# Optimization experiments

Measured on AMD Instinct MI355X. Metric: run time of the kernel, lower is better.

The kernel has to match this reference:

```python
import jax, jax.numpy as jnp
import numpy as np

LOC_SIZE, CID_SIZE, UID_SIZE, TIM_SIZE = 10000, 300, 1000, 48
LOC_EMB, CID_EMB, UID_EMB, TIM_EMB = 256, 64, 64, 32
HID, ENC_HID = 500, 250            # hidden_size, history_hidden_size
SEQ, TGT = 2048, 256
INPUT = LOC_EMB + TIM_EMB + CID_EMB  # 352


def setup_inputs() -> dict:
    key = jax.random.key(0)
    ks = jax.random.split(key, 32)
    n = lambda i, shape, s=0.05: (jax.random.normal(ks[i], shape, dtype=jnp.float32) * s)
    d = {}
    d["loc"] = jax.random.randint(ks[0], (SEQ, 1), 0, LOC_SIZE)
    d["tim"] = jax.random.randint(ks[1], (SEQ, 1), 0, TIM_SIZE)
    d["cid"] = jax.random.randint(ks[2], (SEQ, 1), 0, CID_SIZE)
    d["uid"] = jax.random.randint(ks[3], (1,), 0, UID_SIZE)
    d["target"] = jax.random.randint(ks[4], (TGT, 1), 0, LOC_SIZE)
    d["target_len"] = TGT
    d["time_sim_matrix"] = jax.random.uniform(ks[5], (TIM_SIZE, TIM_SIZE), dtype=jnp.float32)
    # keep distances away from 0 since the model computes 1/dist
    d["poi_distance_matrix"] = jax.random.uniform(ks[6], (LOC_SIZE, LOC_SIZE), dtype=jnp.float32, minval=0.1, maxval=2.0)
    d["poi_cid_tim"] = jax.random.uniform(ks[7], (TIM_SIZE, CID_SIZE), dtype=jnp.float32)
    # embedding tables (emb_loc/emb_cid are pretrained+frozen in the original)
    d["weight"] = n(8, (LOC_SIZE, LOC_EMB))
    d["weight_cid"] = n(9, (CID_SIZE, CID_EMB))
    d["emb_uid_w"] = n(10, (UID_SIZE, UID_EMB))
    d["emb_tim_w"] = n(11, (TIM_SIZE, TIM_EMB))
    # bidirectional encoder LSTM (hidden 250), gate order i,f,g,o like torch
    d["enc_Wih_f"] = n(12, (4 * ENC_HID, INPUT))
    d["enc_Whh_f"] = n(13, (4 * ENC_HID, ENC_HID))
    d["enc_b_f"] = jnp.zeros((4 * ENC_HID,), jnp.float32)
    d["enc_Wih_b"] = n(14, (4 * ENC_HID, INPUT))
    d["enc_Whh_b"] = n(15, (4 * ENC_HID, ENC_HID))
    d["enc_b_b"] = jnp.zeros((4 * ENC_HID,), jnp.float32)
    # decoder LSTM (hidden 500)
    d["dec_Wih"] = n(16, (4 * HID, INPUT))
    d["dec_Whh"] = n(17, (4 * HID, HID))
    d["dec_b"] = jnp.zeros((4 * HID,), jnp.float32)
    # linear layers
    d["fc_user_w"] = n(18, (HID, UID_EMB))
    d["fc_user_b"] = jnp.zeros((HID,), jnp.float32)
    d["fc_final_w"] = n(19, (LOC_SIZE, 3 * HID))
    d["fc_final_b"] = jnp.zeros((LOC_SIZE,), jnp.float32)
    d["fc_final2_w"] = n(20, (HID, 3 * HID))
    d["fc_final2_b"] = jnp.zeros((HID,), jnp.float32)
    return d


def _lstm(x, Wih, Whh, b, H):
    """Single-layer LSTM, batch=1. x: [T, D] -> hs: [T, H]."""
    h0 = jnp.zeros((H,), x.dtype)
    c0 = jnp.zeros((H,), x.dtype)

    def step(carry, xt):
        h, c = carry
        z = Wih @ xt + Whh @ h + b
        i, f, g, o = jnp.split(z, 4)
        c = jax.nn.sigmoid(f) * c + jax.nn.sigmoid(i) * jnp.tanh(g)
        h = jax.nn.sigmoid(o) * jnp.tanh(c)
        return (h, c), h

    _, hs = jax.lax.scan(step, (h0, c0), x)
    return hs


def _table_attn(history, current, table, invert=False, causal=False):
    """Vectorized replacement for the nested-loop lookup attention.
    energies[i, j] = table[current[i], history[j]] (or its reciprocal),
    upper triangle left at 0 for the self-attn variants (as in the original),
    then softmax over the full row (torch F.softmax default dim=1 on 2D)."""
    e = table[current[:, None], history[None, :]]
    if invert:
        e = 1.0 / e
    if causal:
        nn_ = e.shape[0]
        e = jnp.where(jnp.tril(jnp.ones((nn_, nn_), bool)), e, jnp.zeros((), e.dtype))
    return jax.nn.softmax(e, axis=-1)


def reference(loc, tim, cid, uid, target, target_len,
              time_sim_matrix, poi_distance_matrix, poi_cid_tim,
              weight, weight_cid, emb_uid_w, emb_tim_w,
              enc_Wih_f, enc_Whh_f, enc_b_f, enc_Wih_b, enc_Whh_b, enc_b_b,
              dec_Wih, dec_Whh, dec_b,
              fc_user_w, fc_user_b, fc_final_w, fc_final_b, fc_final2_w, fc_final2_b):
    T = int(target_len)
    loc_f, tim_f, cid_f = loc[:, 0], tim[:, 0], cid[:, 0]

    # cross attention: current window attends to history via lookup tables
    attn_cid_time = _table_attn(cid_f[:-T], tim_f[-T:], poi_cid_tim)
    attn_loc = _table_attn(loc_f[:-T], loc_f[-T:], poi_distance_matrix, invert=True)
    attn_time = _table_attn(tim_f[:-T], tim_f[-T:], time_sim_matrix)
    # self attention on the current window (lower-triangular fill)
    self_cid_time = _table_attn(cid_f[-T:], tim_f[-T:], poi_cid_tim, causal=True)
    self_loc = _table_attn(loc_f[-T:], loc_f[-T:], poi_distance_matrix, invert=True, causal=True)
    self_time = _table_attn(tim_f[-T:], tim_f[-T:], time_sim_matrix, causal=True)

    # embeddings (dropout is identity in eval)
    x = jnp.concatenate([weight[loc_f], emb_tim_w[tim_f], weight_cid[cid_f]], axis=1)  # [SEQ, INPUT]
    hist_x, tgt_x = x[:-T], x[-T:]

    # bidirectional encoder over history
    hf = _lstm(hist_x, enc_Wih_f, enc_Whh_f, enc_b_f, ENC_HID)
    hb = _lstm(hist_x[::-1], enc_Wih_b, enc_Whh_b, enc_b_b, ENC_HID)[::-1]
    hidden_history = jnp.concatenate([hf, hb], axis=1)  # [SEQ-T, 2*ENC_HID=500]

    # decoder over current window
    hidden_state = _lstm(tgt_x, dec_Wih, dec_Whh, dec_b, HID)  # [T, 500]

    target_emb = weight[target[:, 0]]  # [T, LOC_EMB]

    uid_emb = emb_uid_w[uid] @ fc_user_w.T + fc_user_b  # [1, 500]
    user_attn = jax.nn.softmax(uid_emb @ hidden_history.T, axis=-1)  # [1, hist]
    context_user = user_attn @ hidden_history  # [1, 500]

    context = (attn_loc + attn_time + attn_cid_time) @ hidden_history  # [T, 500]
    hidden_state = (self_loc + self_time + self_cid_time) @ hidden_state  # [T, 500]

    hidden_state_all = hidden_state + uid_emb  # broadcast of repeat
    out = jnp.concatenate([hidden_state_all, context,
                           jnp.broadcast_to(context_user, (T, HID))], axis=1)  # [T, 1500]
    y = out @ fc_final_w.T + fc_final_b    # [T, LOC_SIZE]
    y1 = out @ fc_final2_w.T + fc_final2_b  # [T, HID]
    score = jax.nn.log_softmax(y, axis=-1)
    return score, y1, target_emb
```

## Files before the change

### kernel.cpp

```cpp
#include <hip/hip_runtime.h>
#include <stdint.h>

#define HIST 1792
#define TGT 256
#define SEQ 2048
#define INPUT 352
#define EHID 250
#define HID 500

typedef _Float16 h2_t __attribute__((ext_vector_type(2)));

static __device__ __forceinline__ float fdot2(uint32_t a, uint32_t b, float c) {
  return __builtin_amdgcn_fdot2(__builtin_bit_cast(h2_t, a),
                                __builtin_bit_cast(h2_t, b), c, false);
}
static __device__ __forceinline__ uint32_t packh2(float lo, float hi) {
  h2_t h; h[0] = (_Float16)lo; h[1] = (_Float16)hi;
  return __builtin_bit_cast(uint32_t, h);
}
static __device__ __forceinline__ uint4 packq(const float* p) {
  uint4 r;
  r.x = packh2(p[0], p[1]); r.y = packh2(p[2], p[3]);
  r.z = packh2(p[4], p[5]); r.w = packh2(p[6], p[7]);
  return r;
}
static __device__ __forceinline__ float dotq(uint4 w, uint4 h, float acc) {
  acc = fdot2(w.x, h.x, acc); acc = fdot2(w.y, h.y, acc);
  acc = fdot2(w.z, h.z, acc); acc = fdot2(w.w, h.w, acc);
  return acc;
}
static __device__ __forceinline__ float sigf(float x) {
  x = fminf(fmaxf(x, -30.f), 30.f);
  return 1.f / (1.f + __expf(-x));
}
static __device__ __forceinline__ float tanh_f(float x) {
  x = fminf(fmaxf(x, -15.f), 15.f);
  float e = __expf(2.f * x);
  return (e - 1.f) / (e + 1.f);
}
static __device__ __forceinline__ void spin_flag(volatile int* f) {
  while (__hip_atomic_load(f, __ATOMIC_ACQUIRE, __HIP_MEMORY_SCOPE_AGENT) == 0)
    __builtin_amdgcn_s_sleep(2);
}
#define AW(dst, src) asm("v_accvgpr_write_b32 %0, %1" : "=a"(dst) : "v"(src))
#define AR(dst, src) asm("v_accvgpr_read_b32 %0, %1" : "=v"(dst) : "a"(src))
#define ARQ(dst, arr, base) do { AR(dst.x, arr[(base)+0]); AR(dst.y, arr[(base)+1]); AR(dst.z, arr[(base)+2]); AR(dst.w, arr[(base)+3]); } while(0)

__global__ void k_embed(const int* __restrict__ loc, const int* __restrict__ tim,
                        const int* __restrict__ cid, const int* __restrict__ target,
                        const float* __restrict__ weight, const float* __restrict__ emb_tim_w,
                        const float* __restrict__ weight_cid,
                        float* __restrict__ x, float* __restrict__ te) {
  int t = blockIdx.x, tid = threadIdx.x;
  if (t < SEQ) {
    int l = loc[t], tm = tim[t], cd = cid[t];
    float* xr = x + (size_t)t * INPUT;
    for (int k = tid; k < 256; k += blockDim.x) xr[k] = weight[(size_t)l * 256 + k];
    for (int k = tid; k < 32; k += blockDim.x)  xr[256 + k] = emb_tim_w[tm * 32 + k];
    for (int k = tid; k < 64; k += blockDim.x)  xr[288 + k] = weight_cid[cd * 64 + k];
  } else {
    int i = t - SEQ;
    int tg = target[i];
    for (int k = tid; k < 256; k += blockDim.x) te[(size_t)i * 256 + k] = weight[(size_t)tg * 256 + k];
  }
}

__global__ void k_gemm_t(const float* __restrict__ A, int lda,
                         const float* __restrict__ W, const float* __restrict__ bias,
                         float* __restrict__ C, int ldc,
                         int M, int N, int K, int revA) {
  __shared__ float As[16][65];
  __shared__ float Ws[16][65];
  const int bn = blockIdx.x * 64, bm = blockIdx.y * 64;
  const int tid = threadIdx.x;
  const int tx = tid & 15, ty = tid >> 4;
  float acc[4][4] = {};
  for (int k0 = 0; k0 < K; k0 += 16) {
    for (int i = tid; i < 1024; i += 256) {
      int m = i >> 4, k = i & 15;
      int gm = bm + m, gk = k0 + k;
      float v = 0.f;
      if (gm < M && gk < K) { int am = revA ? (M - 1 - gm) : gm; v = A[(size_t)am * lda + gk]; }
      As[k][m] = v;
    }
    for (int i = tid; i < 1024; i += 256) {
      int n = i >> 4, k = i & 15;
      int gn = bn + n, gk = k0 + k;
      float v = 0.f;
      if (gn < N && gk < K) v = W[(size_t)gn * K + gk];
      Ws[k][n] = v;
    }
    __syncthreads();
#pragma unroll
    for (int k = 0; k < 16; k++) {
      float a0 = As[k][ty * 4 + 0], a1 = As[k][ty * 4 + 1], a2 = As[k][ty * 4 + 2], a3 = As[k][ty * 4 + 3];
      float b0 = Ws[k][tx * 4 + 0], b1 = Ws[k][tx * 4 + 1], b2 = Ws[k][tx * 4 + 2], b3 = Ws[k][tx * 4 + 3];
      acc[0][0] += a0 * b0; acc[0][1] += a0 * b1; acc[0][2] += a0 * b2; acc[0][3] += a0 * b3;
      acc[1][0] += a1 * b0; acc[1][1] += a1 * b1; acc[1][2] += a1 * b2; acc[1][3] += a1 * b3;
      acc[2][0] += a2 * b0; acc[2][1] += a2 * b1; acc[2][2] += a2 * b2; acc[2][3] += a2 * b3;
      acc[3][0] += a3 * b0; acc[3][1] += a3 * b1; acc[3][2] += a3 * b2; acc[3][3] += a3 * b3;
    }
    __syncthreads();
  }
  for (int i = 0; i < 4; i++) {
    int gm = bm + ty * 4 + i; if (gm >= M) continue;
    for (int j = 0; j < 4; j++) {
      int gn = bn + tx * 4 + j; if (gn >= N) continue;
      C[(size_t)gm * ldc + gn] = acc[i][j] + (bias ? bias[gn] : 0.f);
    }
  }
}

__global__ void k_gemm_nn(const float* __restrict__ A, int lda,
                          const float* __restrict__ B, int ldb,
                          const float* __restrict__ addvec,
                          float* __restrict__ C, int ldc,
                          int M, int N, int K) {
  __shared__ float As[16][65];
  __shared__ float Bs[16][65];
  const int bn = blockIdx.x * 64, bm = blockIdx.y * 64;
  const int tid = threadIdx.x;
  const int tx = tid & 15, ty = tid >> 4;
  float acc[4][4] = {};
  for (int k0 = 0; k0 < K; k0 += 16) {
    for (int i = tid; i < 1024; i += 256) {
      int m = i >> 4, k = i & 15;
      int gm = bm + m, gk = k0 + k;
      float v = 0.f;
      if (gm < M && gk < K) v = A[(size_t)gm * lda + gk];
      As[k][m] = v;
    }
    for (int i = tid; i < 1024; i += 256) {
      int k = i >> 6, n = i & 63;
      int gk = k0 + k, gn = bn + n;
      float v = 0.f;
      if (gk < K && gn < N) v = B[(size_t)gk * ldb + gn];
      Bs[k][n] = v;
    }
    __syncthreads();
#pragma unroll
    for (int k = 0; k < 16; k++) {
      float a0 = As[k][ty * 4 + 0], a1 = As[k][ty * 4 + 1], a2 = As[k][ty * 4 + 2], a3 = As[k][ty * 4 + 3];
      float b0 = Bs[k][tx * 4 + 0], b1 = Bs[k][tx * 4 + 1], b2 = Bs[k][tx * 4 + 2], b3 = Bs[k][tx * 4 + 3];
      acc[0][0] += a0 * b0; acc[0][1] += a0 * b1; acc[0][2] += a0 * b2; acc[0][3] += a0 * b3;
      acc[1][0] += a1 * b0; acc[1][1] += a1 * b1; acc[1][2] += a1 * b2; acc[1][3] += a1 * b3;
      acc[2][0] += a2 * b0; acc[2][1] += a2 * b1; acc[2][2] += a2 * b2; acc[2][3] += a2 * b3;
      acc[3][0] += a3 * b0; acc[3][1] += a3 * b1; acc[3][2] += a3 * b2; acc[3][3] += a3 * b3;
    }
    __syncthreads();
  }
  for (int i = 0; i < 4; i++) {
    int gm = bm + ty * 4 + i; if (gm >= M) continue;
    for (int j = 0; j < 4; j++) {
      int gn = bn + tx * 4 + j; if (gn >= N) continue;
      C[(size_t)gm * ldc + gn] = acc[i][j] + (addvec ? addvec[gn] : 0.f);
    }
  }
}

#define WQL 12
#define WBYTES (WQL * 512 * 16)
__launch_bounds__(512)
__global__ void k_lstm(const float* __restrict__ A_f, const float* __restrict__ A_b,
                       const float* __restrict__ A_d,
                       const float* __restrict__ Whh_f, const float* __restrict__ Whh_b,
                       const float* __restrict__ Whh_d,
                       float* __restrict__ hh, float* __restrict__ hdec,
                       float* zpub, uint32_t* hpub, int* flag_z, int* flag_h) {
  const int b = blockIdx.x;
  const int tid = threadIdx.x;
  __shared__ __align__(16) unsigned char smem[WBYTES + 2048 + 4096];
  uint4* wl = (uint4*)smem;
  uint4* hbuf = (uint4*)(smem + WBYTES);
  float* zbuf = (float*)(smem + WBYTES + 2048);

  if (tid < 128) hbuf[tid] = make_uint4(0, 0, 0, 0);

  if (b < 2) {
    const float* A = (b == 0) ? A_f : A_b;
    const float* Whh = (b == 0) ? Whh_f : Whh_b;
    const bool act = tid < 500;
    uint4 wv0[10], wv1[10];
    uint32_t wa[128];
    if (act) {
      const float* wr0 = Whh + (size_t)tid * EHID;
      const float* wr1 = Whh + (size_t)(tid + 500) * EHID;
#pragma unroll
      for (int q = 0; q < 6; q++) {
        float t0[8], t1[8];
#pragma unroll
        for (int cc = 0; cc < 8; cc++) {
          int col = 208 + 8 * q + cc;
          t0[cc] = (col < EHID) ? wr0[col] : 0.f;
          t1[cc] = (col < EHID) ? wr1[col] : 0.f;
        }
        wl[(q * 2 + 0) * 512 + tid] = packq(t0);
        wl[(q * 2 + 1) * 512 + tid] = packq(t1);
      }
#pragma unroll
      for (int k = 0; k < 16; k++) {
        uint4 p0 = packq(wr0 + 8 * (10 + k));
        uint4 p1 = packq(wr1 + 8 * (10 + k));
        AW(wa[k * 4 + 0], p0.x); AW(wa[k * 4 + 1], p0.y);
        AW(wa[k * 4 + 2], p0.z); AW(wa[k * 4 + 3], p0.w);
        AW(wa[64 + k * 4 + 0], p1.x); AW(wa[64 + k * 4 + 1], p1.y);
        AW(wa[64 + k * 4 + 2], p1.z); AW(wa[64 + k * 4 + 3], p1.w);
      }
#pragma unroll
      for (int q = 0; q < 10; q++) { wv0[q] = packq(wr0 + 8 * q); wv1[q] = packq(wr1 + 8 * q); }
    }
    float c = 0.f;
    float aA = act ? A[tid] : 0.f;
    float aB = act ? A[500 + tid] : 0.f;
    __syncthreads();
    for (int t = 0; t < HIST; t++) {
      const uint4* hb = hbuf + (t & 1) * 32;
      if (act) {
        float z0 = aA, z1 = aB, y0 = 0.f, y1 = 0.f;
        int tn = (t + 1 < HIST) ? t + 1 : t;
        aA = A[tn * 1000 + tid];
        aB = A[tn * 1000 + 500 + tid];
#pragma unroll
        for (int q = 0; q < 10; q++) {
          uint4 hq = hb[q];
          z0 = dotq(wv0[q], hq, z0);
          z1 = dotq(wv1[q], hq, z1);
        }
#pragma unroll
        for (int k = 0; k < 16; k++) {
          uint4 hq = hb[10 + k];
          uint4 u0, u1;
          ARQ(u0, wa, k * 4);
          ARQ(u1, wa, 64 + k * 4);
          y0 = dotq(u0, hq, y0);
          y1 = dotq(u1, hq, y1);
        }
#pragma unroll
        for (int q = 0; q < 6; q++) {
          uint4 hq = hb[26 + q];
          z0 = dotq(wl[(q * 2 + 0) * 512 + tid], hq, z0);
          z1 = dotq(wl[(q * 2 + 1) * 512 + tid], hq, z1);
        }
        zbuf[tid] = z0 + y0;
        zbuf[500 + tid] = z1 + y1;
      }
      __syncthreads();
      float hval = 0.f;
      if (tid < EHID) {
        float zi = zbuf[tid], zf = zbuf[250 + tid], zg = zbuf[500 + tid], zo = zbuf[750 + tid];
        c = sigf(zf) * c + sigf(zi) * tanh_f(zg);
        hval = sigf(zo) * tanh_f(c);
        if (b == 0) hh[(size_t)t * HID + tid] = hval;
        else        hh[(size_t)(HIST - 1 - t) * HID + EHID + tid] = hval;
      }
      float hother = __shfl_xor(hval, 1);
      uint32_t* hw = (uint32_t*)(hbuf + ((t + 1) & 1) * 32);
      if (tid < EHID && !(tid & 1)) hw[tid >> 1] = packh2(hval, hother);
      __syncthreads();
    }
  } else {
    const int gi = b - 2;
    const int j = tid;
    const bool act = (j < 500);
    uint4 wv[20];
    uint32_t wa[128];
    if (act) {
      const float* wr = Whh_d + (size_t)(gi * 500 + j) * HID;
#pragma unroll
      for (int q = 0; q < 12; q++) {
        float tmp[8];
#pragma unroll
        for (int cc = 0; cc < 8; cc++) {
          int col = 416 + 8 * q + cc;
          tmp[cc] = (col < HID) ? wr[col] : 0.f;
        }
        wl[q * 512 + tid] = packq(tmp);
      }
#pragma unroll
      for (int k = 0; k < 32; k++) {
        uint4 pq = packq(wr + 8 * (20 + k));
        AW(wa[k * 4 + 0], pq.x); AW(wa[k * 4 + 1], pq.y);
        AW(wa[k * 4 + 2], pq.z); AW(wa[k * 4 + 3], pq.w);
      }
#pragma unroll
      for (int q = 0; q < 20; q++) wv[q] = packq(wr + 8 * q);
    }
    uint32_t* hdd = (uint32_t*)hbuf;
    float c = 0.f;
    float aD = act ? A_d[gi * 500 + j] : 0.f;
    __syncthreads();
    for (int t = 0; t < TGT; t++) {
      const uint4* hb = hbuf + (t & 1) * 64;
      float z = 0.f;
      if (act) {
        float z0 = aD, z1 = 0.f, z2 = 0.f, z3 = 0.f;
        int tn = (t + 1 < TGT) ? t + 1 : t;
        aD = A_d[tn * 2000 + gi * 500 + j];
#pragma unroll
        for (int q = 0; q < 20; q += 2) {
          z0 = dotq(wv[q], hb[q], z0);
          z1 = dotq(wv[q + 1], hb[q + 1], z1);
        }
#pragma unroll
        for (int k = 0; k < 32; k += 2) {
          uint4 u0, u1;
          ARQ(u0, wa, k * 4);
          ARQ(u1, wa, (k + 1) * 4);
          z2 = dotq(u0, hb[20 + k], z2);
          z3 = dotq(u1, hb[21 + k], z3);
        }
#pragma unroll
        for (int q = 0; q < 12; q += 2) {
          z0 = dotq(wl[q * 512 + tid], hb[52 + q], z0);
          z1 = dotq(wl[(q + 1) * 512 + tid], hb[53 + q], z1);
        }
        z = (z0 + z1) + (z2 + z3);
      }
      if (gi < 3) {
        if (act) zpub[gi * 512 + j] = z;
        __threadfence();
        __syncthreads();
        if (tid == 0) {
          __hip_atomic_store(&flag_z[t * 3 + gi], 1, __ATOMIC_RELEASE, __HIP_MEMORY_SCOPE_AGENT);
          spin_flag(&flag_h[t]);
        }
        __syncthreads();
        uint32_t* hw = (uint32_t*)(hbuf + ((t + 1) & 1) * 64);
        if (tid < 250)
          hw[tid] = __hip_atomic_load(&hpub[tid], __ATOMIC_RELAXED, __HIP_MEMORY_SCOPE_AGENT);
        __syncthreads();
      } else {
        if (tid == 0) {
          spin_flag(&flag_z[t * 3 + 0]);
          spin_flag(&flag_z[t * 3 + 1]);
          spin_flag(&flag_z[t * 3 + 2]);
        }
        __syncthreads();
        float hval = 0.f;
        if (act) {
          float zi = __hip_atomic_load(&zpub[0 * 512 + j], __ATOMIC_RELAXED, __HIP_MEMORY_SCOPE_AGENT);
          float zf = __hip_atomic_load(&zpub[1 * 512 + j], __ATOMIC_RELAXED, __HIP_MEMORY_SCOPE_AGENT);
          float zg = __hip_atomic_load(&zpub[2 * 512 + j], __ATOMIC_RELAXED, __HIP_MEMORY_SCOPE_AGENT);
          c = sigf(zf) * c + sigf(zi) * tanh_f(zg);
          hval = sigf(z) * tanh_f(c);
          hdec[(size_t)t * HID + j] = hval;
        }
        float hother = __shfl_xor(hval, 1);
        uint32_t* hw = (uint32_t*)(hbuf + ((t + 1) & 1) * 64);
        if (act && !(j & 1)) {
          uint32_t p = packh2(hval, hother);
          hw[j >> 1] = p;
          __hip_atomic_store(&hpub[j >> 1], p, __ATOMIC_RELAXED, __HIP_MEMORY_SCOPE_AGENT);
        }
        __threadfence();
        __syncthreads();
        if (tid == 0)
          __hip_atomic_store(&flag_h[t], 1, __ATOMIC_RELEASE, __HIP_MEMORY_SCOPE_AGENT);
      }
    }
  }
}

__global__ void k_attn(const int* __restrict__ loc, const int* __restrict__ tim,
                       const int* __restrict__ cid,
                       const float* __restrict__ ts, const float* __restrict__ pd,
                       const float* __restrict__ pct,
                       float* __restrict__ S1, float* __restrict__ S2) {
  const int i = blockIdx.x;
  const int tid = threadIdx.x;
  __shared__ float e[HIST];
  __shared__ float red[256];
  const int loc_i = loc[HIST + i], tim_i = tim[HIST + i];
  for (int tab = 0; tab < 3; tab++) {
    for (int jj = tid; jj < HIST; jj += 256) {
      float v;
      if (tab == 0)      v = 1.f / pd[(size_t)loc_i * 10000 + loc[jj]];
      else if (tab == 1) v = ts[tim_i * 48 + tim[jj]];
      else               v = pct[tim_i * 300 + cid[jj]];
      e[jj] = v;
    }
    __syncthreads();
    float mx = -1e30f;
    for (int jj = tid; jj < HIST; jj += 256) mx = fmaxf(mx, e[jj]);
    red[tid] = mx; __syncthreads();
    for (int s = 128; s > 0; s >>= 1) { if (tid < s) red[tid] = fmaxf(red[tid], red[tid + s]); __syncthreads(); }
    mx = red[0]; __syncthreads();
    float sm = 0.f;
    for (int jj = tid; jj < HIST; jj += 256) sm += __expf(e[jj] - mx);
    red[tid] = sm; __syncthreads();
    for (int s = 128; s > 0; s >>= 1) { if (tid < s) red[tid] += red[tid + s]; __syncthreads(); }
    float inv = 1.f / red[0]; __syncthreads();
    for (int jj = tid; jj < HIST; jj += 256) {
      float p = __expf(e[jj] - mx) * inv;
      if (tab == 0) S1[(size_t)i * HIST + jj] = p; else S1[(size_t)i * HIST + jj] += p;
    }
    __syncthreads();
  }
  const int lj = loc[HIST + tid], tj = tim[HIST + tid], cj = cid[HIST + tid];
  for (int tab = 0; tab < 3; tab++) {
    float v;
    if (tab == 0)      v = 1.f / pd[(size_t)loc_i * 10000 + lj];
    else if (tab == 1) v = ts[tim_i * 48 + tj];
    else               v = pct[tim_i * 300 + cj];
    if (tid > i) v = 0.f;
    red[tid] = v; __syncthreads();
    for (int s = 128; s > 0; s >>= 1) { if (tid < s) red[tid] = fmaxf(red[tid], red[tid + s]); __syncthreads(); }
    float mx = red[0]; __syncthreads();
    float ex = __expf(v - mx);
    red[tid] = ex; __syncthreads();
    for (int s = 128; s > 0; s >>= 1) { if (tid < s) red[tid] += red[tid + s]; __syncthreads(); }
    float p = ex / red[0]; __syncthreads();
    if (tab == 0) S2[(size_t)i * TGT + tid] = p; else S2[(size_t)i * TGT + tid] += p;
    __syncthreads();
  }
}

__global__ void k_uid(const int* __restrict__ uid, const float* __restrict__ emb_uid_w,
                      const float* __restrict__ fc_user_w, const float* __restrict__ fc_user_b,
                      float* __restrict__ uid_emb) {
  const int tid = threadIdx.x;
  __shared__ float u[64];
  if (tid < 64) u[tid] = emb_uid_w[(size_t)uid[0] * 64 + tid];
  __syncthreads();
  if (tid < HID) {
    float a = fc_user_b[tid];
    for (int k = 0; k < 64; k++) a += u[k] * fc_user_w[tid * 64 + k];
    uid_emb[tid] = a;
  }
}

__global__ void k_user(const float* __restrict__ uid_emb, const float* __restrict__ hh,
                       float* __restrict__ out) {
  const int tid = threadIdx.x;
  __shared__ float s[HIST];
  __shared__ float red[1024];
  __shared__ float ue[HID];
  if (tid < HID) ue[tid] = uid_emb[tid];
  __syncthreads();
  for (int t = tid; t < HIST; t += 1024) {
    float a = 0.f;
    const float* hr = hh + (size_t)t * HID;
    for (int k = 0; k < HID; k++) a += ue[k] * hr[k];
    s[t] = a;
  }
  __syncthreads();
  float mx = -1e30f;
  for (int t = tid; t < HIST; t += 1024) mx = fmaxf(mx, s[t]);
  red[tid] = mx; __syncthreads();
  for (int st = 512; st > 0; st >>= 1) { if (tid < st) red[tid] = fmaxf(red[tid], red[tid + st]); __syncthreads(); }
  mx = red[0]; __syncthreads();
  float sm = 0.f;
  for (int t = tid; t < HIST; t += 1024) sm += __expf(s[t] - mx);
  red[tid] = sm; __syncthreads();
  for (int st = 512; st > 0; st >>= 1) { if (tid < st) red[tid] += red[tid + st]; __syncthreads(); }
  float inv = 1.f / red[0]; __syncthreads();
  for (int t = tid; t < HIST; t += 1024) s[t] = __expf(s[t] - mx) * inv;
  __syncthreads();
  if (tid < HID) {
    float a = 0.f;
    for (int t = 0; t < HIST; t++) a += s[t] * hh[(size_t)t * HID + tid];
    for (int i = 0; i < TGT; i++) out[(size_t)i * 1500 + 1000 + tid] = a;
  }
}

__global__ void k_logsoftmax(float* __restrict__ y) {
  const int i = blockIdx.x;
  const int tid = threadIdx.x;
  float* r = y + (size_t)i * 10000;
  __shared__ float red[1024];
  float mx = -1e30f;
  for (int j = tid; j < 10000; j += 1024) mx = fmaxf(mx, r[j]);
  red[tid] = mx; __syncthreads();
  for (int s = 512; s > 0; s >>= 1) { if (tid < s) red[tid] = fmaxf(red[tid], red[tid + s]); __syncthreads(); }
  mx = red[0]; __syncthreads();
  float sm = 0.f;
  for (int j = tid; j < 10000; j += 1024) sm += __expf(r[j] - mx);
  red[tid] = sm; __syncthreads();
  for (int s = 512; s > 0; s >>= 1) { if (tid < s) red[tid] += red[tid + s]; __syncthreads(); }
  float lse = mx + __logf(red[0]);
  __syncthreads();
  for (int j = tid; j < 10000; j += 1024) r[j] = r[j] - lse;
}

extern "C" void kernel_launch(void* const* d_in, const int* in_sizes, int n_in,
                              void* d_out, int out_size, void* d_ws, size_t ws_size,
                              hipStream_t stream) {
  (void)in_sizes; (void)n_in; (void)out_size; (void)ws_size;
  const int* loc = (const int*)d_in[0];
  const int* tim = (const int*)d_in[1];
  const int* cid = (const int*)d_in[2];
  const int* uid = (const int*)d_in[3];
  const int* target = (const int*)d_in[4];
  const float* ts = (const float*)d_in[6];
  const float* pd = (const float*)d_in[7];
  const float* pct = (const float*)d_in[8];
  const float* weight = (const float*)d_in[9];
  const float* weight_cid = (const float*)d_in[10];
  const float* emb_uid_w = (const float*)d_in[11];
  const float* emb_tim_w = (const float*)d_in[12];
  const float* enc_Wih_f = (const float*)d_in[13];
  const float* enc_Whh_f = (const float*)d_in[14];
  const float* enc_b_f = (const float*)d_in[15];
  const float* enc_Wih_b = (const float*)d_in[16];
  const float* enc_Whh_b = (const float*)d_in[17];
  const float* enc_b_b = (const float*)d_in[18];
  const float* dec_Wih = (const float*)d_in[19];
  const float* dec_Whh = (const float*)d_in[20];
  const float* dec_b = (const float*)d_in[21];
  const float* fc_user_w = (const float*)d_in[22];
  const float* fc_user_b = (const float*)d_in[23];
  const float* fc_final_w = (const float*)d_in[24];
  const float* fc_final_b = (const float*)d_in[25];
  const float* fc_final2_w = (const float*)d_in[26];
  const float* fc_final2_b = (const float*)d_in[27];

  float* score = (float*)d_out;
  float* y1 = score + (size_t)TGT * 10000;
  float* te = y1 + (size_t)TGT * HID;

  float* ws = (float*)d_ws;
  float* x = ws;
  float* A_f = x + (size_t)SEQ * INPUT;
  float* A_b = A_f + (size_t)HIST * 1000;
  float* A_d = A_b + (size_t)HIST * 1000;
  float* hh = A_d + (size_t)TGT * 2000;
  float* hdec = hh + (size_t)HIST * HID;
  float* S1 = hdec + (size_t)TGT * HID;
  float* S2 = S1 + (size_t)TGT * HIST;
  float* outb = S2 + (size_t)TGT * TGT;
  float* uid_emb = outb + (size_t)TGT * 1500;
  float* zpub = uid_emb + 512;
  uint32_t* hpub = (uint32_t*)(zpub + 3 * 512);
  int* flag_z = (int*)(hpub + 256);
  int* flag_h = flag_z + 3 * TGT;

  k_embed<<<dim3(SEQ + TGT), dim3(128), 0, stream>>>(loc, tim, cid, target, weight, emb_tim_w, weight_cid, x, te);

  k_gemm_t<<<dim3(16, 28), dim3(256), 0, stream>>>(x, INPUT, enc_Wih_f, enc_b_f, A_f, 1000, HIST, 1000, INPUT, 0);
  k_gemm_t<<<dim3(16, 28), dim3(256), 0, stream>>>(x, INPUT, enc_Wih_b, enc_b_b, A_b, 1000, HIST, 1000, INPUT, 1);
  k_gemm_t<<<dim3(32, 4), dim3(256), 0, stream>>>(x + (size_t)HIST * INPUT, INPUT, dec_Wih, dec_b, A_d, 2000, TGT, 2000, INPUT, 0);

  hipMemsetAsync(flag_z, 0, 4 * TGT * sizeof(int), stream);

  k_attn<<<dim3(TGT), dim3(256), 0, stream>>>(loc, tim, cid, ts, pd, pct, S1, S2);
  k_uid<<<dim3(1), dim3(512), 0, stream>>>(uid, emb_uid_w, fc_user_w, fc_user_b, uid_emb);

  k_lstm<<<dim3(6), dim3(512), 0, stream>>>(A_f, A_b, A_d, enc_Whh_f, enc_Whh_b, dec_Whh,
                                            hh, hdec, zpub, hpub, flag_z, flag_h);

  k_user<<<dim3(1), dim3(1024), 0, stream>>>(uid_emb, hh, outb);
  k_gemm_nn<<<dim3(8, 4), dim3(256), 0, stream>>>(S2, TGT, hdec, HID, uid_emb, outb, 1500, TGT, HID, TGT);
  k_gemm_nn<<<dim3(8, 4), dim3(256), 0, stream>>>(S1, HIST, hh, HID, nullptr, outb + 500, 1500, TGT, HID, HIST);

  k_gemm_t<<<dim3(157, 4), dim3(256), 0, stream>>>(outb, 1500, fc_final_w, fc_final_b, score, 10000, TGT, 10000, 1500, 0);
  k_gemm_t<<<dim3(8, 4), dim3(256), 0, stream>>>(outb, 1500, fc_final2_w, fc_final2_b, y1, 500, TGT, 500, 1500, 0);

  k_logsoftmax<<<dim3(TGT), dim3(1024), 0, stream>>>(score);
}
```

Before: 5.369 ms.

## Use fp16 dot2 in GEMMs and shuffle-based gate exchange in encoder LSTM

GEMM kernels now pack operands to fp16 pairs in shared memory and accumulate with fdot2, halving shared traffic and inner-loop instructions. The encoder LSTM maps each cell's four gate rows onto a thread pair and exchanges gate pre-activations via lane shuffles, removing the shared z buffer and one block barrier per timestep. This trades precision in the GEMMs (fp16 inputs) for throughput and shortens the serial recurrence step.

```diff
diff --git a/kernel.cpp b/kernel.cpp
--- a/kernel.cpp
+++ b/kernel.cpp
@@ -65,40 +65,51 @@
   }
 }
 
-__global__ void k_gemm_t(const float* __restrict__ A, int lda,
-                         const float* __restrict__ W, const float* __restrict__ bias,
-                         float* __restrict__ C, int ldc,
-                         int M, int N, int K, int revA) {
-  __shared__ float As[16][65];
-  __shared__ float Ws[16][65];
+__global__ void k_gemm_t16(const float* __restrict__ A, int lda,
+                           const float* __restrict__ W, const float* __restrict__ bias,
+                           float* __restrict__ C, int ldc,
+                           int M, int N, int K, int revA) {
+  __shared__ uint32_t AsP[8][65];
+  __shared__ uint32_t WsP[8][65];
   const int bn = blockIdx.x * 64, bm = blockIdx.y * 64;
   const int tid = threadIdx.x;
   const int tx = tid & 15, ty = tid >> 4;
   float acc[4][4] = {};
   for (int k0 = 0; k0 < K; k0 += 16) {
-    for (int i = tid; i < 1024; i += 256) {
-      int m = i >> 4, k = i & 15;
-      int gm = bm + m, gk = k0 + k;
-      float v = 0.f;
-      if (gm < M && gk < K) { int am = revA ? (M - 1 - gm) : gm; v = A[(size_t)am * lda + gk]; }
-      As[k][m] = v;
-    }
-    for (int i = tid; i < 1024; i += 256) {
-      int n = i >> 4, k = i & 15;
-      int gn = bn + n, gk = k0 + k;
-      float v = 0.f;
-      if (gn < N && gk < K) v = W[(size_t)gn * K + gk];
-      Ws[k][n] = v;
-    }
-    __syncthreads();
-#pragma unroll
-    for (int k = 0; k < 16; k++) {
-      float a0 = As[k][ty * 4 + 0], a1 = As[k][ty * 4 + 1], a2 = As[k][ty * 4 + 2], a3 = As[k][ty * 4 + 3];
-      float b0 = Ws[k][tx * 4 + 0], b1 = Ws[k][tx * 4 + 1], b2 = Ws[k][tx * 4 + 2], b3 = Ws[k][tx * 4 + 3];
-      acc[0][0] += a0 * b0; acc[0][1] += a0 * b1; acc[0][2] += a0 * b2; acc[0][3] += a0 * b3;
-      acc[1][0] += a1 * b0; acc[1][1] += a1 * b1; acc[1][2] += a1 * b2; acc[1][3] += a1 * b3;
-      acc[2][0] += a2 * b0; acc[2][1] += a2 * b1; acc[2][2] += a2 * b2; acc[2][3] += a2 * b3;
-      acc[3][0] += a3 * b0; acc[3][1] += a3 * b1; acc[3][2] += a3 * b2; acc[3][3] += a3 * b3;
+    for (int i = tid; i < 512; i += 256) {
+      int m = i & 63, kk = i >> 6;
+      int gm = bm + m, gk = k0 + 2 * kk;
+      float v0 = 0.f, v1 = 0.f;
+      if (gm < M) {
+        int am = revA ? (M - 1 - gm) : gm;
+        if (gk < K)     v0 = A[(size_t)am * lda + gk];
+        if (gk + 1 < K) v1 = A[(size_t)am * lda + gk + 1];
+      }
+      AsP[kk][m] = packh2(v0, v1);
+    }
+    for (int i = tid; i < 512; i += 256) {
+      int n = i & 63, kk = i >> 6;
+      int gn = bn + n, gk = k0 + 2 * kk;
+      float v0 = 0.f, v1 = 0.f;
+      if (gn < N) {
+        if (gk < K)     v0 = W[(size_t)gn * K + gk];
+        if (gk + 1 < K) v1 = W[(size_t)gn * K + gk + 1];
+      }
+      WsP[kk][n] = packh2(v0, v1);
+    }
+    __syncthreads();
+#pragma unroll
+    for (int kk = 0; kk < 8; kk++) {
+      uint32_t a0 = AsP[kk][ty * 4 + 0], a1 = AsP[kk][ty * 4 + 1], a2 = AsP[kk][ty * 4 + 2], a3 = AsP[kk][ty * 4 + 3];
+      uint32_t b0 = WsP[kk][tx * 4 + 0], b1 = WsP[kk][tx * 4 + 1], b2 = WsP[kk][tx * 4 + 2], b3 = WsP[kk][tx * 4 + 3];
+      acc[0][0] = fdot2(a0, b0, acc[0][0]); acc[0][1] = fdot2(a0, b1, acc[0][1]);
+      acc[0][2] = fdot2(a0, b2, acc[0][2]); acc[0][3] = fdot2(a0, b3, acc[0][3]);
+      acc[1][0] = fdot2(a1, b0, acc[1][0]); acc[1][1] = fdot2(a1, b1, acc[1][1]);
+      acc[1][2] = fdot2(a1, b2, acc[1][2]); acc[1][3] = fdot2(a1, b3, acc[1][3]);
+      acc[2][0] = fdot2(a2, b0, acc[2][0]); acc[2][1] = fdot2(a2, b1, acc[2][1]);
+      acc[2][2] = fdot2(a2, b2, acc[2][2]); acc[2][3] = fdot2(a2, b3, acc[2][3]);
+      acc[3][0] = fdot2(a3, b0, acc[3][0]); acc[3][1] = fdot2(a3, b1, acc[3][1]);
+      acc[3][2] = fdot2(a3, b2, acc[3][2]); acc[3][3] = fdot2(a3, b3, acc[3][3]);
     }
     __syncthreads();
   }
@@ -111,41 +122,51 @@
   }
 }
 
-__global__ void k_gemm_nn(const float* __restrict__ A, int lda,
-                          const float* __restrict__ B, int ldb,
-                          const float* __restrict__ addvec,
-                          float* __restrict__ C, int ldc,
-                          int M, int N, int K) {
-  __shared__ float As[16][65];
-  __shared__ float Bs[16][65];
+__global__ void k_gemm_nn16(const float* __restrict__ A, int lda,
+                            const float* __restrict__ B, int ldb,
+                            const float* __restrict__ addvec,
+                            float* __restrict__ C, int ldc,
+                            int M, int N, int K) {
+  __shared__ uint32_t AsP[8][65];
+  __shared__ uint32_t BsP[8][65];
   const int bn = blockIdx.x * 64, bm = blockIdx.y * 64;
   const int tid = threadIdx.x;
   const int tx = tid & 15, ty = tid >> 4;
   float acc[4][4] = {};
   for (int k0 = 0; k0 < K; k0 += 16) {
-    for (int i = tid; i < 1024; i += 256) {
-      int m = i >> 4, k = i & 15;
-      int gm = bm + m, gk = k0 + k;
-      float v = 0.f;
-      if (gm < M && gk < K) v = A[(size_t)gm * lda + gk];
-      As[k][m] = v;
-    }
-    for (int i = tid; i < 1024; i += 256) {
-      int k = i >> 6, n = i & 63;
-      int gk = k0 + k, gn = bn + n;
-      float v = 0.f;
-      if (gk < K && gn < N) v = B[(size_t)gk * ldb + gn];
-      Bs[k][n] = v;
-    }
-    __syncthreads();
-#pragma unroll
-    for (int k = 0; k < 16; k++) {
-      float a0 = As[k][ty * 4 + 0], a1 = As[k][ty * 4 + 1], a2 = As[k][ty * 4 + 2], a3 = As[k][ty * 4 + 3];
-      float b0 = Bs[k][tx * 4 + 0], b1 = Bs[k][tx * 4 + 1], b2 = Bs[k][tx * 4 + 2], b3 = Bs[k][tx * 4 + 3];
-      acc[0][0] += a0 * b0; acc[0][1] += a0 * b1; acc[0][2] += a0 * b2; acc[0][3] += a0 * b3;
-      acc[1][0] += a1 * b0; acc[1][1] += a1 * b1; acc[1][2] += a1 * b2; acc[1][3] += a1 * b3;
-      acc[2][0] += a2 * b0; acc[2][1] += a2 * b1; acc[2][2] += a2 * b2; acc[2][3] += a2 * b3;
-      acc[3][0] += a3 * b0; acc[3][1] += a3 * b1; acc[3][2] += a3 * b2; acc[3][3] += a3 * b3;
+    for (int i = tid; i < 512; i += 256) {
+      int m = i & 63, kk = i >> 6;
+      int gm = bm + m, gk = k0 + 2 * kk;
+      float v0 = 0.f, v1 = 0.f;
+      if (gm < M) {
+        if (gk < K)     v0 = A[(size_t)gm * lda + gk];
+        if (gk + 1 < K) v1 = A[(size_t)gm * lda + gk + 1];
+      }
+      AsP[kk][m] = packh2(v0, v1);
+    }
+    for (int i = tid; i < 512; i += 256) {
+      int n = i & 63, kk = i >> 6;
+      int gn = bn + n, gk = k0 + 2 * kk;
+      float v0 = 0.f, v1 = 0.f;
+      if (gn < N) {
+        if (gk < K)     v0 = B[(size_t)gk * ldb + gn];
+        if (gk + 1 < K) v1 = B[(size_t)(gk + 1) * ldb + gn];
+      }
+      BsP[kk][n] = packh2(v0, v1);
+    }
+    __syncthreads();
+#pragma unroll
+    for (int kk = 0; kk < 8; kk++) {
+      uint32_t a0 = AsP[kk][ty * 4 + 0], a1 = AsP[kk][ty * 4 + 1], a2 = AsP[kk][ty * 4 + 2], a3 = AsP[kk][ty * 4 + 3];
+      uint32_t b0 = BsP[kk][tx * 4 + 0], b1 = BsP[kk][tx * 4 + 1], b2 = BsP[kk][tx * 4 + 2], b3 = BsP[kk][tx * 4 + 3];
+      acc[0][0] = fdot2(a0, b0, acc[0][0]); acc[0][1] = fdot2(a0, b1, acc[0][1]);
+      acc[0][2] = fdot2(a0, b2, acc[0][2]); acc[0][3] = fdot2(a0, b3, acc[0][3]);
+      acc[1][0] = fdot2(a1, b0, acc[1][0]); acc[1][1] = fdot2(a1, b1, acc[1][1]);
+      acc[1][2] = fdot2(a1, b2, acc[1][2]); acc[1][3] = fdot2(a1, b3, acc[1][3]);
+      acc[2][0] = fdot2(a2, b0, acc[2][0]); acc[2][1] = fdot2(a2, b1, acc[2][1]);
+      acc[2][2] = fdot2(a2, b2, acc[2][2]); acc[2][3] = fdot2(a2, b3, acc[2][3]);
+      acc[3][0] = fdot2(a3, b0, acc[3][0]); acc[3][1] = fdot2(a3, b1, acc[3][1]);
+      acc[3][2] = fdot2(a3, b2, acc[3][2]); acc[3][3] = fdot2(a3, b3, acc[3][3]);
     }
     __syncthreads();
   }
@@ -169,10 +190,9 @@
                        float* zpub, uint32_t* hpub, int* flag_z, int* flag_h) {
   const int b = blockIdx.x;
   const int tid = threadIdx.x;
-  __shared__ __align__(16) unsigned char smem[WBYTES + 2048 + 4096];
+  __shared__ __align__(16) unsigned char smem[WBYTES + 2048];
   uint4* wl = (uint4*)smem;
   uint4* hbuf = (uint4*)(smem + WBYTES);
-  float* zbuf = (float*)(smem + WBYTES + 2048);
 
   if (tid < 128) hbuf[tid] = make_uint4(0, 0, 0, 0);
 
@@ -180,11 +200,15 @@
     const float* A = (b == 0) ? A_f : A_b;
     const float* Whh = (b == 0) ? Whh_f : Whh_b;
     const bool act = tid < 500;
+    const int cell = act ? (tid >> 1) : 249;
+    const int role = tid & 1;
+    const int row0 = role * 250 + cell;
+    const int row1 = 500 + role * 250 + cell;
     uint4 wv0[10], wv1[10];
     uint32_t wa[128];
     if (act) {
-      const float* wr0 = Whh + (size_t)tid * EHID;
-      const float* wr1 = Whh + (size_t)(tid + 500) * EHID;
+      const float* wr0 = Whh + (size_t)row0 * EHID;
+      const float* wr1 = Whh + (size_t)row1 * EHID;
 #pragma unroll
       for (int q = 0; q < 6; q++) {
         float t0[8], t1[8];
@@ -210,16 +234,17 @@
       for (int q = 0; q < 10; q++) { wv0[q] = packq(wr0 + 8 * q); wv1[q] = packq(wr1 + 8 * q); }
     }
     float c = 0.f;
-    float aA = act ? A[tid] : 0.f;
-    float aB = act ? A[500 + tid] : 0.f;
+    float aA = act ? A[row0] : 0.f;
+    float aB = act ? A[row1] : 0.f;
     __syncthreads();
     for (int t = 0; t < HIST; t++) {
       const uint4* hb = hbuf + (t & 1) * 32;
+      float z_r0 = 0.f, z_r1 = 0.f;
       if (act) {
         float z0 = aA, z1 = aB, y0 = 0.f, y1 = 0.f;
         int tn = (t + 1 < HIST) ? t + 1 : t;
-        aA = A[tn * 1000 + tid];
-        aB = A[tn * 1000 + 500 + tid];
+        aA = A[tn * 1000 + row0];
+        aB = A[tn * 1000 + row1];
 #pragma unroll
         for (int q = 0; q < 10; q++) {
           uint4 hq = hb[q];
@@ -241,21 +266,27 @@
           z0 = dotq(wl[(q * 2 + 0) * 512 + tid], hq, z0);
           z1 = dotq(wl[(q * 2 + 1) * 512 + tid], hq, z1);
         }
-        zbuf[tid] = z0 + y0;
-        zbuf[500 + tid] = z1 + y1;
-      }
-      __syncthreads();
+        z_r0 = z0 + y0;
+        z_r1 = z1 + y1;
+      }
+      float pA = __shfl_xor(z_r0, 1);
+      float pB = __shfl_xor(z_r1, 1);
+      float zi = role ? pA : z_r0;
+      float zf = role ? z_r0 : pA;
+      float zg = role ? pB : z_r1;
+      float zo = role ? z_r1 : pB;
       float hval = 0.f;
-      if (tid < EHID) {
-        float zi = zbuf[tid], zf = zbuf[250 + tid], zg = zbuf[500 + tid], zo = zbuf[750 + tid];
+      if (act) {
         c = sigf(zf) * c + sigf(zi) * tanh_f(zg);
         hval = sigf(zo) * tanh_f(c);
-        if (b == 0) hh[(size_t)t * HID + tid] = hval;
-        else        hh[(size_t)(HIST - 1 - t) * HID + EHID + tid] = hval;
-      }
-      float hother = __shfl_xor(hval, 1);
+        if (role == 0) {
+          if (b == 0) hh[(size_t)t * HID + cell] = hval;
+          else        hh[(size_t)(HIST - 1 - t) * HID + EHID + cell] = hval;
+        }
+      }
+      float hn = __shfl_xor(hval, 2);
       uint32_t* hw = (uint32_t*)(hbuf + ((t + 1) & 1) * 32);
-      if (tid < EHID && !(tid & 1)) hw[tid >> 1] = packh2(hval, hother);
+      if (act && (tid & 3) == 0) hw[tid >> 2] = packh2(hval, hn);
       __syncthreads();
     }
   } else {
@@ -285,7 +316,6 @@
 #pragma unroll
       for (int q = 0; q < 20; q++) wv[q] = packq(wr + 8 * q);
     }
-    uint32_t* hdd = (uint32_t*)hbuf;
     float c = 0.f;
     float aD = act ? A_d[gi * 500 + j] : 0.f;
     __syncthreads();
@@ -536,9 +566,9 @@
 
   k_embed<<<dim3(SEQ + TGT), dim3(128), 0, stream>>>(loc, tim, cid, target, weight, emb_tim_w, weight_cid, x, te);
 
-  k_gemm_t<<<dim3(16, 28), dim3(256), 0, stream>>>(x, INPUT, enc_Wih_f, enc_b_f, A_f, 1000, HIST, 1000, INPUT, 0);
-  k_gemm_t<<<dim3(16, 28), dim3(256), 0, stream>>>(x, INPUT, enc_Wih_b, enc_b_b, A_b, 1000, HIST, 1000, INPUT, 1);
-  k_gemm_t<<<dim3(32, 4), dim3(256), 0, stream>>>(x + (size_t)HIST * INPUT, INPUT, dec_Wih, dec_b, A_d, 2000, TGT, 2000, INPUT, 0);
+  k_gemm_t16<<<dim3(16, 28), dim3(256), 0, stream>>>(x, INPUT, enc_Wih_f, enc_b_f, A_f, 1000, HIST, 1000, INPUT, 0);
+  k_gemm_t16<<<dim3(16, 28), dim3(256), 0, stream>>>(x, INPUT, enc_Wih_b, enc_b_b, A_b, 1000, HIST, 1000, INPUT, 1);
+  k_gemm_t16<<<dim3(32, 4), dim3(256), 0, stream>>>(x + (size_t)HIST * INPUT, INPUT, dec_Wih, dec_b, A_d, 2000, TGT, 2000, INPUT, 0);
 
   hipMemsetAsync(flag_z, 0, 4 * TGT * sizeof(int), stream);
 
@@ -549,11 +579,11 @@
                                             hh, hdec, zpub, hpub, flag_z, flag_h);
 
   k_user<<<dim3(1), dim3(1024), 0, stream>>>(uid_emb, hh, outb);
-  k_gemm_nn<<<dim3(8, 4), dim3(256), 0, stream>>>(S2, TGT, hdec, HID, uid_emb, outb, 1500, TGT, HID, TGT);
-  k_gemm_nn<<<dim3(8, 4), dim3(256), 0, stream>>>(S1, HIST, hh, HID, nullptr, outb + 500, 1500, TGT, HID, HIST);
-
-  k_gemm_t<<<dim3(157, 4), dim3(256), 0, stream>>>(outb, 1500, fc_final_w, fc_final_b, score, 10000, TGT, 10000, 1500, 0);
-  k_gemm_t<<<dim3(8, 4), dim3(256), 0, stream>>>(outb, 1500, fc_final2_w, fc_final2_b, y1, 500, TGT, 500, 1500, 0);
+  k_gemm_nn16<<<dim3(8, 4), dim3(256), 0, stream>>>(S2, TGT, hdec, HID, uid_emb, outb, 1500, TGT, HID, TGT);
+  k_gemm_nn16<<<dim3(8, 4), dim3(256), 0, stream>>>(S1, HIST, hh, HID, nullptr, outb + 500, 1500, TGT, HID, HIST);
+
+  k_gemm_t16<<<dim3(157, 4), dim3(256), 0, stream>>>(outb, 1500, fc_final_w, fc_final_b, score, 10000, TGT, 10000, 1500, 0);
+  k_gemm_t16<<<dim3(8, 4), dim3(256), 0, stream>>>(outb, 1500, fc_final2_w, fc_final2_b, y1, 500, TGT, 500, 1500, 0);
 
   k_logsoftmax<<<dim3(TGT), dim3(1024), 0, stream>>>(score);
 }
```

Result: no change. 5.433 ms (+1.2%).
